# Kernel tuning notes

Hardware: AMD Instinct MI355X
Metric: run time of the kernel (lower is better)

## Reference

```python
import jax, jax.numpy as jnp
import numpy as np

DIM = 384
NUM_HEADS = 12
HEAD_DIM = DIM // NUM_HEADS  # 32
SCALE = HEAD_DIM ** -0.5
B, N = 4, 2048


def setup_inputs() -> dict:
    key = jax.random.key(0)
    k0, k1, k2, k3 = jax.random.split(key, 4)
    x = jax.random.normal(k0, (B, N, DIM), dtype=jnp.float32)
    # nn.Linear(dim, 3*dim, bias=False): y = x @ W_qkv, W_qkv is [C, 3C]
    W_qkv = jax.random.normal(k1, (DIM, 3 * DIM), dtype=jnp.float32) * (DIM ** -0.5)
    # nn.Linear(dim, dim): y = x @ W_proj + b_proj, W_proj is [C, C]
    W_proj = jax.random.normal(k2, (DIM, DIM), dtype=jnp.float32) * (DIM ** -0.5)
    b_proj = jax.random.normal(k3, (DIM,), dtype=jnp.float32) * 0.01
    return {"x": x, "W_qkv": W_qkv, "W_proj": W_proj, "b_proj": b_proj}


def reference(x, W_qkv, W_proj, b_proj):
    b, n, c = x.shape
    qkv = (x @ W_qkv).reshape(b, n, 3, NUM_HEADS, HEAD_DIM)
    qkv = jnp.transpose(qkv, (2, 0, 3, 1, 4))  # [3, B, H, N, hd]
    q, k, v = qkv[0], qkv[1], qkv[2]
    # full attention: softmax(q k^T * scale) v
    attn = jnp.einsum('bhqd,bhkd->bhqk', q, k) * SCALE  # [B,H,N,N]
    attn = jax.nn.softmax(attn, axis=-1)
    out = jnp.einsum('bhqk,bhkd->bhqd', attn, v)  # [B,H,N,hd]
    out = jnp.transpose(out, (0, 2, 1, 3)).reshape(b, n, c)
    return out @ W_proj + b_proj
```

## Files before the change

### kernel.cpp

```cpp
#include <hip/hip_runtime.h>

constexpr int BB  = 4;
constexpr int SEQ = 2048;
constexpr int CC  = 384;
constexpr int C3  = 1152;
constexpr int NH  = 12;
constexpr int HD  = 32;
constexpr float SCALE = 0.17677669529663689f;
constexpr float LOG2E = 1.4426950408889634f;
constexpr size_t KV_BYTES = (size_t)2 * BB * NH * SEQ * HD * 2;
constexpr size_t WT_BYTES = ((size_t)C3 * CC + (size_t)CC * CC) * 2;
constexpr size_t XB_BYTES = (size_t)BB * SEQ * CC * 2;

typedef __attribute__((ext_vector_type(8))) short short8_t;
typedef __attribute__((ext_vector_type(4))) float floatx4;

#if __has_builtin(__builtin_amdgcn_exp2f)
#define EXP2F __builtin_amdgcn_exp2f
#else
#define EXP2F __builtin_exp2f
#endif

__device__ __forceinline__ unsigned short f2bf(float f) {
    unsigned int u = __builtin_bit_cast(unsigned int, f);
    u += 0x7fffu + ((u >> 16) & 1u);
    return (unsigned short)(u >> 16);
}
__device__ __forceinline__ unsigned int pk_rn(float lo, float hi) {
    return __builtin_amdgcn_perm(__builtin_bit_cast(unsigned int, hi) + 0x8000u,
                                 __builtin_bit_cast(unsigned int, lo) + 0x8000u,
                                 0x07060302u);
}
__device__ __forceinline__ short8_t pack8(float4 a, float4 b) {
    uint4 u;
    u.x = pk_rn(a.x, a.y); u.y = pk_rn(a.z, a.w);
    u.z = pk_rn(b.x, b.y); u.w = pk_rn(b.z, b.w);
    return __builtin_bit_cast(short8_t, u);
}

__global__ __launch_bounds__(256) void prep_kernel(
    const float* __restrict__ x, const float* __restrict__ wqkv,
    const float* __restrict__ wproj,
    unsigned short* __restrict__ wqkvT, unsigned short* __restrict__ wprojT,
    unsigned short* __restrict__ xb)
{
    const int bid = blockIdx.x;
    if (bid >= 144) {
        const size_t base = (size_t)(bid - 144) * 2048 + threadIdx.x * 8;
        const float4 a = *(const float4*)(x + base);
        const float4 b = *(const float4*)(x + base + 4);
        uint4 u;
        u.x = pk_rn(a.x, a.y); u.y = pk_rn(a.z, a.w);
        u.z = pk_rn(b.x, b.y); u.w = pk_rn(b.z, b.w);
        *(uint4*)(xb + base) = u;
        return;
    }
    __shared__ float ls[64][68];
    const float* src; unsigned short* dst; int SN, k0, n0;
    if (bid < 108) {
        src = wqkv; dst = wqkvT; SN = C3;
        k0 = (bid / 18) * 64; n0 = (bid % 18) * 64;
    } else {
        const int b2 = bid - 108;
        src = wproj; dst = wprojT; SN = CC;
        k0 = (b2 / 6) * 64; n0 = (b2 % 6) * 64;
    }
    const int t  = threadIdx.x;
    const int rr = t >> 4, cc4 = (t & 15) * 4;
#pragma unroll
    for (int p = 0; p < 4; ++p) {
        const int row = p * 16 + rr;
        const float4 v = *(const float4*)&src[(size_t)(k0 + row) * SN + n0 + cc4];
        ls[row][cc4] = v.x; ls[row][cc4 + 1] = v.y;
        ls[row][cc4 + 2] = v.z; ls[row][cc4 + 3] = v.w;
    }
    __syncthreads();
#pragma unroll
    for (int p = 0; p < 4; ++p) {
        const int nrow = p * 16 + rr;
        uint2 u;
        u.x = pk_rn(ls[cc4][nrow],     ls[cc4 + 1][nrow]);
        u.y = pk_rn(ls[cc4 + 2][nrow], ls[cc4 + 3][nrow]);
        *(uint2*)&dst[(size_t)(n0 + nrow) * CC + k0 + cc4] = u;
    }
}

__global__ __launch_bounds__(256) void qkv_fast(
    const unsigned short* __restrict__ xb,
    const unsigned short* __restrict__ wT,
    float* __restrict__ dq,
    unsigned short* __restrict__ kv)
{
    __shared__ __align__(16) unsigned short As[2][128][40];
    __shared__ __align__(16) unsigned short Bs[2][128][40];

    const int mt   = blockIdx.x & 63;
    const int nb   = blockIdx.x >> 6;
    const int tid  = threadIdx.x;
    const int wid  = tid >> 6;
    const int lane = tid & 63;
    const int quad = lane >> 4;
    const int col  = lane & 15;
    const int wr   = wid >> 1, wc = wid & 1;
    const int m0 = mt * 128, n0 = nb * 128;

    const int arow = tid >> 1;
    const int aoff = (tid & 1) * 16;

    floatx4 acc[4][4];
#pragma unroll
    for (int i = 0; i < 4; ++i)
#pragma unroll
        for (int j = 0; j < 4; ++j) acc[i][j] = (floatx4){0.f, 0.f, 0.f, 0.f};

    const unsigned short* xrow = xb + (size_t)(m0 + arow) * CC + aoff;
    const unsigned short* wrow = wT + (size_t)(n0 + arow) * CC + aoff;

    short8_t ast0, ast1, bst0, bst1;
    ast0 = *(const short8_t*)xrow;
    ast1 = *(const short8_t*)(xrow + 8);
    bst0 = *(const short8_t*)wrow;
    bst1 = *(const short8_t*)(wrow + 8);
    *(short8_t*)&As[0][arow][aoff]     = ast0;
    *(short8_t*)&As[0][arow][aoff + 8] = ast1;
    *(short8_t*)&Bs[0][arow][aoff]     = bst0;
    *(short8_t*)&Bs[0][arow][aoff + 8] = bst1;

    for (int it = 0; it < CC / 32; ++it) {
        const int kn = (it + 1 < CC / 32) ? (it + 1) * 32 : 0;
        ast0 = *(const short8_t*)(xrow + kn);
        ast1 = *(const short8_t*)(xrow + kn + 8);
        bst0 = *(const short8_t*)(wrow + kn);
        bst1 = *(const short8_t*)(wrow + kn + 8);

        __syncthreads();
        const int p = it & 1;
        short8_t af[4], bf[4];
#pragma unroll
        for (int i = 0; i < 4; ++i)
            af[i] = *(const short8_t*)&As[p][wr * 64 + i * 16 + col][quad * 8];
#pragma unroll
        for (int j = 0; j < 4; ++j)
            bf[j] = *(const short8_t*)&Bs[p][wc * 64 + j * 16 + col][quad * 8];
#pragma unroll
        for (int j = 0; j < 4; ++j)
#pragma unroll
            for (int i = 0; i < 4; ++i)
                acc[i][j] = __builtin_amdgcn_mfma_f32_16x16x32_bf16(af[i], bf[j], acc[i][j], 0, 0, 0);

        *(short8_t*)&As[p ^ 1][arow][aoff]     = ast0;
        *(short8_t*)&As[p ^ 1][arow][aoff + 8] = ast1;
        *(short8_t*)&Bs[p ^ 1][arow][aoff]     = bst0;
        *(short8_t*)&Bs[p ^ 1][arow][aoff + 8] = bst1;
    }

    const int t = nb / 3;
#pragma unroll
    for (int i = 0; i < 4; ++i) {
        const int mg = m0 + wr * 64 + i * 16 + quad * 4;
        if (t == 0) {
#pragma unroll
            for (int j = 0; j < 4; ++j) {
                const int n = n0 + wc * 64 + j * 16 + col;
#pragma unroll
                for (int r = 0; r < 4; ++r)
                    dq[(size_t)(mg + r) * CC + n] = acc[i][j][r];
            }
        } else if (t == 1) {
            const int b = mg >> 11, s = mg & (SEQ - 1);
#pragma unroll
            for (int j = 0; j < 4; ++j) {
                const int rem = n0 - CC + wc * 64 + j * 16 + col;
                const int h = rem >> 5, d = rem & 31;
                unsigned short* kp = kv + ((size_t)(b * NH + h) * SEQ + s) * HD + d;
#pragma unroll
                for (int r = 0; r < 4; ++r)
                    kp[(size_t)r * HD] = f2bf(acc[i][j][r]);
            }
        } else {
            const int b = mg >> 11, s = mg & (SEQ - 1);
            unsigned short* vtb = kv + (size_t)BB * NH * SEQ * HD;
#pragma unroll
            for (int j = 0; j < 4; ++j) {
                const int rem = n0 - 2 * CC + wc * 64 + j * 16 + col;
                const int h = rem >> 5, d = rem & 31;
                uint2 u;
                u.x = pk_rn(acc[i][j][0], acc[i][j][1]);
                u.y = pk_rn(acc[i][j][2], acc[i][j][3]);
                *(uint2*)&vtb[((size_t)(b * NH + h) * HD + d) * SEQ + s] = u;
            }
        }
    }
}

__global__ __launch_bounds__(256) void attn_kernel(
    const unsigned short* __restrict__ kv,
    float* qatt)
{
    const int bid  = blockIdx.x;
    const int qp   = bid / 48;
    const int bh   = bid % 48;
    const int h    = bh % NH;
    const int b    = bh / NH;
    const int w    = threadIdx.x >> 6;
    const int lane = threadIdx.x & 63;
    const int quad = lane >> 4;
    const int col  = lane & 15;
    const int tid  = threadIdx.x;

    const unsigned short* K  = kv + (size_t)bh * SEQ * HD;
    const unsigned short* VT = kv + (size_t)BB * NH * SEQ * HD + (size_t)bh * HD * SEQ;

    __shared__ __align__(16) unsigned short Kt[2][128][40];
    __shared__ __align__(16) unsigned short Vt[2][32][136];

    const int krow_s = tid >> 1, koff_s = (tid & 1) * 16;
    const int drow_s = tid >> 3, voff_s = (tid & 7) * 16;

    int qrow[2];
    short8_t qf[2];
    const float sc = SCALE * LOG2E;
#pragma unroll
    for (int t = 0; t < 2; ++t) {
        qrow[t] = b * SEQ + qp * 128 + (w + 4 * t) * 16 + col;
        const float* qpt = qatt + (size_t)qrow[t] * CC + h * HD + quad * 8;
        const float4 a0 = *(const float4*)qpt;
        const float4 a1 = *(const float4*)(qpt + 4);
        const float4 s0 = {a0.x * sc, a0.y * sc, a0.z * sc, a0.w * sc};
        const float4 s1 = {a1.x * sc, a1.y * sc, a1.z * sc, a1.w * sc};
        qf[t] = pack8(s0, s1);
    }

    short8_t ones;
#pragma unroll
    for (int e = 0; e < 8; ++e) ones[e] = (short)0x3F80;

    floatx4 o[2][2];
    floatx4 lacc[2];
#pragma unroll
    for (int t = 0; t < 2; ++t) {
        lacc[t] = (floatx4){0.f, 0.f, 0.f, 0.f};
#pragma unroll
        for (int i = 0; i < 2; ++i) o[t][i] = (floatx4){0.f, 0.f, 0.f, 0.f};
    }
    const float ci = -10.f * LOG2E;
    const floatx4 cinit = {ci, ci, ci, ci};

    short8_t k0a = *(const short8_t*)(K + (size_t)krow_s * HD + koff_s);
    short8_t k0b = *(const short8_t*)(K + (size_t)krow_s * HD + koff_s + 8);
    short8_t v0a = *(const short8_t*)(VT + (size_t)drow_s * SEQ + voff_s);
    short8_t v0b = *(const short8_t*)(VT + (size_t)drow_s * SEQ + voff_s + 8);
    *(short8_t*)&Kt[0][krow_s][koff_s]     = k0a;
    *(short8_t*)&Kt[0][krow_s][koff_s + 8] = k0b;
    *(short8_t*)&Vt[0][drow_s][voff_s]     = v0a;
    *(short8_t*)&Vt[0][drow_s][voff_s + 8] = v0b;

    for (int it = 0; it < SEQ / 128; ++it) {
        const int kn = ((it + 1) * 128) & (SEQ - 1);
        k0a = *(const short8_t*)(K + (size_t)(kn + krow_s) * HD + koff_s);
        k0b = *(const short8_t*)(K + (size_t)(kn + krow_s) * HD + koff_s + 8);
        v0a = *(const short8_t*)(VT + (size_t)drow_s * SEQ + kn + voff_s);
        v0b = *(const short8_t*)(VT + (size_t)drow_s * SEQ + kn + voff_s + 8);

        __syncthreads();
        const int p = it & 1;

#pragma unroll
        for (int c = 0; c < 4; ++c) {
            const int c32 = c * 32;
            const short8_t ka0 = *(const short8_t*)&Kt[p][c32 + col][quad * 8];
            const short8_t ka1 = *(const short8_t*)&Kt[p][c32 + 16 + col][quad * 8];
            const uint2 w0a = *(const uint2*)&Vt[p][col][c32 + quad * 4];
            const uint2 w0b = *(const uint2*)&Vt[p][col][c32 + 16 + quad * 4];
            const uint2 w1a = *(const uint2*)&Vt[p][16 + col][c32 + quad * 4];
            const uint2 w1b = *(const uint2*)&Vt[p][16 + col][c32 + 16 + quad * 4];
            const short8_t va0 = __builtin_bit_cast(short8_t, (uint4){w0a.x, w0a.y, w0b.x, w0b.y});
            const short8_t va1 = __builtin_bit_cast(short8_t, (uint4){w1a.x, w1a.y, w1b.x, w1b.y});
#pragma unroll
            for (int t = 0; t < 2; ++t) {
                const floatx4 s0 = __builtin_amdgcn_mfma_f32_16x16x32_bf16(ka0, qf[t], cinit, 0, 0, 0);
                const floatx4 s1 = __builtin_amdgcn_mfma_f32_16x16x32_bf16(ka1, qf[t], cinit, 0, 0, 0);
                const float p00 = EXP2F(s0[0]), p01 = EXP2F(s0[1]);
                const float p02 = EXP2F(s0[2]), p03 = EXP2F(s0[3]);
                const float p10 = EXP2F(s1[0]), p11 = EXP2F(s1[1]);
                const float p12 = EXP2F(s1[2]), p13 = EXP2F(s1[3]);
                const uint4 pu = {pk_rn(p00, p01), pk_rn(p02, p03),
                                  pk_rn(p10, p11), pk_rn(p12, p13)};
                const short8_t pb = __builtin_bit_cast(short8_t, pu);
                o[t][0] = __builtin_amdgcn_mfma_f32_16x16x32_bf16(va0, pb, o[t][0], 0, 0, 0);
                o[t][1] = __builtin_amdgcn_mfma_f32_16x16x32_bf16(va1, pb, o[t][1], 0, 0, 0);
                lacc[t] = __builtin_amdgcn_mfma_f32_16x16x32_bf16(ones, pb, lacc[t], 0, 0, 0);
            }
        }

        *(short8_t*)&Kt[p ^ 1][krow_s][koff_s]     = k0a;
        *(short8_t*)&Kt[p ^ 1][krow_s][koff_s + 8] = k0b;
        *(short8_t*)&Vt[p ^ 1][drow_s][voff_s]     = v0a;
        *(short8_t*)&Vt[p ^ 1][drow_s][voff_s + 8] = v0b;
    }

#pragma unroll
    for (int t = 0; t < 2; ++t) {
        const float inv = 1.f / lacc[t][0];
        float* op = qatt + (size_t)qrow[t] * CC + h * HD;
#pragma unroll
        for (int r = 0; r < 4; ++r) {
            op[quad * 4 + r]      = o[t][0][r] * inv;
            op[16 + quad * 4 + r] = o[t][1][r] * inv;
        }
    }
}

__global__ __launch_bounds__(256) void proj_fast(
    float* att,
    const unsigned short* __restrict__ wT,
    const float* __restrict__ bias)
{
    __shared__ __align__(16) unsigned short Bs[2][384][32];
    __shared__ __align__(16) unsigned short As[2][32][40];

    const int mt   = blockIdx.x;
    const int tid  = threadIdx.x;
    const int wid  = tid >> 6;
    const int lane = tid & 63;
    const int quad = lane >> 4;
    const int col  = lane & 15;
    const int m0   = mt * 32;

    const int arow = tid >> 3, akoff = (tid & 7) * 4;

    floatx4 acc[2][6];
#pragma unroll
    for (int i = 0; i < 2; ++i)
#pragma unroll
        for (int j = 0; j < 6; ++j) acc[i][j] = (floatx4){0.f, 0.f, 0.f, 0.f};

    short8_t bst[3][2];
    uint2 asr;
    {
#pragma unroll
        for (int j = 0; j < 3; ++j) {
            const int f = j * 256 + tid;
            const unsigned short* wp = wT + (size_t)(f >> 1) * CC + (f & 1) * 16;
            bst[j][0] = *(const short8_t*)wp;
            bst[j][1] = *(const short8_t*)(wp + 8);
        }
        const float4 av = *(const float4*)(att + (size_t)(m0 + arow) * CC + akoff);
        asr = (uint2){pk_rn(av.x, av.y), pk_rn(av.z, av.w)};
#pragma unroll
        for (int j = 0; j < 3; ++j) {
            const int f = j * 256 + tid;
            *(short8_t*)&Bs[0][f >> 1][(f & 1) * 16]     = bst[j][0];
            *(short8_t*)&Bs[0][f >> 1][(f & 1) * 16 + 8] = bst[j][1];
        }
        *(uint2*)&As[0][arow][akoff] = asr;
    }

    for (int it = 0; it < CC / 32; ++it) {
        const int kn = (it + 1 < CC / 32) ? (it + 1) * 32 : 0;
#pragma unroll
        for (int j = 0; j < 3; ++j) {
            const int f = j * 256 + tid;
            const unsigned short* wp = wT + (size_t)(f >> 1) * CC + kn + (f & 1) * 16;
            bst[j][0] = *(const short8_t*)wp;
            bst[j][1] = *(const short8_t*)(wp + 8);
        }
        const float4 av = *(const float4*)(att + (size_t)(m0 + arow) * CC + kn + akoff);
        asr = (uint2){pk_rn(av.x, av.y), pk_rn(av.z, av.w)};

        __syncthreads();
        const int p = it & 1;
        short8_t af[2], bf[6];
#pragma unroll
        for (int i = 0; i < 2; ++i)
            af[i] = *(const short8_t*)&As[p][i * 16 + col][quad * 8];
#pragma unroll
        for (int j = 0; j < 6; ++j)
            bf[j] = *(const short8_t*)&Bs[p][wid * 96 + j * 16 + col][quad * 8];
#pragma unroll
        for (int j = 0; j < 6; ++j)
#pragma unroll
            for (int i = 0; i < 2; ++i)
                acc[i][j] = __builtin_amdgcn_mfma_f32_16x16x32_bf16(af[i], bf[j], acc[i][j], 0, 0, 0);

#pragma unroll
        for (int j = 0; j < 3; ++j) {
            const int f = j * 256 + tid;
            *(short8_t*)&Bs[p ^ 1][f >> 1][(f & 1) * 16]     = bst[j][0];
            *(short8_t*)&Bs[p ^ 1][f >> 1][(f & 1) * 16 + 8] = bst[j][1];
        }
        *(uint2*)&As[p ^ 1][arow][akoff] = asr;
    }

    __syncthreads();
#pragma unroll
    for (int j = 0; j < 6; ++j) {
        const int n = wid * 96 + j * 16 + col;
        const float bv = bias[n];
#pragma unroll
        for (int i = 0; i < 2; ++i)
#pragma unroll
            for (int r = 0; r < 4; ++r)
                att[(size_t)(m0 + i * 16 + quad * 4 + r) * CC + n] = acc[i][j][r] + bv;
    }
}

__global__ __launch_bounds__(256) void qkv_lds(
    const float* __restrict__ x, const float* __restrict__ w,
    float* __restrict__ dq, unsigned short* __restrict__ kv)
{
    __shared__ __align__(16) unsigned short wt[128 * 40];
    const int mt = blockIdx.x & 63, nb = blockIdx.x >> 6;
    const int tid = threadIdx.x, wid = tid >> 6, lane = tid & 63;
    const int quad = lane >> 4, col = lane & 15;
    const int wr = wid >> 1, wc = wid & 1;
    const int m0 = mt * 128, n0 = nb * 128;
    const int sn = tid >> 1, skg = (tid & 1) * 4;

    floatx4 acc[4][4];
#pragma unroll
    for (int i = 0; i < 4; ++i)
#pragma unroll
        for (int j = 0; j < 4; ++j) acc[i][j] = (floatx4){0.f, 0.f, 0.f, 0.f};
    const float* xbase = x + (size_t)(m0 + wr * 64 + col) * CC;

    for (int kb = 0; kb < CC; kb += 32) {
        float wv[4][4];
#pragma unroll
        for (int s = 0; s < 4; ++s) {
            const int k = kb + (skg + s) * 4;
#pragma unroll
            for (int j = 0; j < 4; ++j) wv[s][j] = w[(size_t)(k + j) * C3 + n0 + sn];
        }
        short8_t af[4];
#pragma unroll
        for (int i = 0; i < 4; ++i) {
            const float* xr = xbase + (size_t)i * 16 * CC + kb + quad * 8;
            af[i] = pack8(*(const float4*)xr, *(const float4*)(xr + 4));
        }
        __syncthreads();
#pragma unroll
        for (int s = 0; s < 4; ++s) {
            ushort4 u;
            u.x = f2bf(wv[s][0]); u.y = f2bf(wv[s][1]);
            u.z = f2bf(wv[s][2]); u.w = f2bf(wv[s][3]);
            *(ushort4*)&wt[sn * 40 + (skg + s) * 4] = u;
        }
        __syncthreads();
#pragma unroll
        for (int j = 0; j < 4; ++j) {
            const short8_t bf = *(const short8_t*)&wt[(wc * 64 + j * 16 + col) * 40 + quad * 8];
#pragma unroll
            for (int i = 0; i < 4; ++i)
                acc[i][j] = __builtin_amdgcn_mfma_f32_16x16x32_bf16(af[i], bf, acc[i][j], 0, 0, 0);
        }
    }
    const int t = nb / 3;
#pragma unroll
    for (int i = 0; i < 4; ++i) {
        const int mg = m0 + wr * 64 + i * 16 + quad * 4;
        if (t == 0) {
#pragma unroll
            for (int j = 0; j < 4; ++j) {
                const int n = n0 + wc * 64 + j * 16 + col;
#pragma unroll
                for (int r = 0; r < 4; ++r) dq[(size_t)(mg + r) * CC + n] = acc[i][j][r];
            }
        } else if (t == 1) {
            const int b = mg >> 11, s = mg & (SEQ - 1);
#pragma unroll
            for (int j = 0; j < 4; ++j) {
                const int rem = n0 - CC + wc * 64 + j * 16 + col;
                const int h = rem >> 5, d = rem & 31;
                unsigned short* kp = kv + ((size_t)(b * NH + h) * SEQ + s) * HD + d;
#pragma unroll
                for (int r = 0; r < 4; ++r) kp[(size_t)r * HD] = f2bf(acc[i][j][r]);
            }
        } else {
            const int b = mg >> 11, s = mg & (SEQ - 1);
            unsigned short* vtb = kv + (size_t)BB * NH * SEQ * HD;
#pragma unroll
            for (int j = 0; j < 4; ++j) {
                const int rem = n0 - 2 * CC + wc * 64 + j * 16 + col;
                const int h = rem >> 5, d = rem & 31;
                uint2 u;
                u.x = pk_rn(acc[i][j][0], acc[i][j][1]);
                u.y = pk_rn(acc[i][j][2], acc[i][j][3]);
                *(uint2*)&vtb[((size_t)(b * NH + h) * HD + d) * SEQ + s] = u;
            }
        }
    }
}

__global__ __launch_bounds__(256) void proj_lds(
    float* att, const float* __restrict__ wp, const float* __restrict__ bias)
{
    __shared__ __align__(16) unsigned short wt[CC * 40];
    const int mt = blockIdx.x, tid = threadIdx.x, wid = tid >> 6, lane = tid & 63;
    const int quad = lane >> 4, col = lane & 15;
    const int m0 = mt * 16;
    floatx4 acc[6];
#pragma unroll
    for (int j = 0; j < 6; ++j) acc[j] = (floatx4){0.f, 0.f, 0.f, 0.f};
    for (int kb = 0; kb < CC; kb += 32) {
        float gv[12][4];
#pragma unroll
        for (int g = 0; g < 12; ++g) {
            const int flat = tid + g * 256, n = flat % 384, kg = flat / 384;
#pragma unroll
            for (int j = 0; j < 4; ++j) gv[g][j] = wp[(size_t)(kb + kg * 4 + j) * CC + n];
        }
        __syncthreads();
#pragma unroll
        for (int g = 0; g < 12; ++g) {
            const int flat = tid + g * 256, n = flat % 384, kg = flat / 384;
            ushort4 u;
            u.x = f2bf(gv[g][0]); u.y = f2bf(gv[g][1]);
            u.z = f2bf(gv[g][2]); u.w = f2bf(gv[g][3]);
            *(ushort4*)&wt[n * 40 + kg * 4] = u;
        }
        __syncthreads();
        const float* ap = att + (size_t)(m0 + col) * CC + kb + quad * 8;
        const short8_t af = pack8(*(const float4*)ap, *(const float4*)(ap + 4));
#pragma unroll
        for (int j = 0; j < 6; ++j) {
            const short8_t pb = *(const short8_t*)&wt[(wid * 96 + j * 16 + col) * 40 + quad * 8];
            acc[j] = __builtin_amdgcn_mfma_f32_16x16x32_bf16(af, pb, acc[j], 0, 0, 0);
        }
    }
    __syncthreads();
#pragma unroll
    for (int j = 0; j < 6; ++j) {
        const int n = wid * 96 + j * 16 + col;
        const float bv = bias[n];
#pragma unroll
        for (int r = 0; r < 4; ++r)
            att[(size_t)(m0 + quad * 4 + r) * CC + n] = acc[j][r] + bv;
    }
}

__global__ void marker_kernel(float* out, float val, int nelem) {
    int i = blockIdx.x * 256 + threadIdx.x;
    if (i < nelem) out[i] = val;
}

extern "C" void kernel_launch(void* const* d_in, const int* in_sizes, int n_in,
                              void* d_out, int out_size, void* d_ws, size_t ws_size,
                              hipStream_t stream)
{
    const float* x     = (const float*)d_in[0];
    const float* wqkv  = (const float*)d_in[1];
    const float* wproj = (const float*)d_in[2];
    const float* bproj = (const float*)d_in[3];
    float* out = (float*)d_out;
    unsigned short* kv = (unsigned short*)d_ws;

    if (ws_size < KV_BYTES) {
        const float marker = 100.f + (float)(ws_size >> 20);
        marker_kernel<<<(out_size + 255) / 256, 256, 0, stream>>>(out, marker, out_size);
        return;
    }

    unsigned short* wqkvT  = kv + (size_t)2 * BB * NH * SEQ * HD;
    unsigned short* wprojT = wqkvT + (size_t)C3 * CC;
    unsigned short* xb     = wprojT + (size_t)CC * CC;

    if (ws_size >= KV_BYTES + WT_BYTES + XB_BYTES) {
        prep_kernel<<<144 + 1536, 256, 0, stream>>>(x, wqkv, wproj, wqkvT, wprojT, xb);
        qkv_fast<<<576, 256, 0, stream>>>(xb, wqkvT, out, kv);
        attn_kernel<<<16 * BB * NH, 256, 0, stream>>>(kv, out);
        proj_fast<<<BB * SEQ / 32, 256, 0, stream>>>(out, wprojT, bproj);
    } else {
        qkv_lds<<<576, 256, 0, stream>>>(x, wqkv, out, kv);
        attn_kernel<<<16 * BB * NH, 256, 0, stream>>>(kv, out);
        proj_lds<<<BB * SEQ / 16, 256, 0, stream>>>(out, wproj, bproj);
    }
}
```

Measured before the change: 143.3 us.

## Store Q and attention output as bf16 intermediates, fold softmax scale into K

The QKV GEMM now writes Q as bf16 into the output buffer instead of fp32. The softmax scale is folded into K at write time. The attention kernel reads bf16 Q directly and writes its output as bf16 into the xb workspace, so proj_fast loads A fragments straight from global memory with no LDS staging or fp32-to-bf16 conversion. This halves the intermediate traffic and removes a shared-memory buffer and one barrier, at the cost of rounding Q before the scale is applied and keeping a duplicate fp32 attention kernel for the fallback path.

```diff
diff --git a/kernel.cpp b/kernel.cpp
--- a/kernel.cpp
+++ b/kernel.cpp
@@ -8,6 +8,7 @@
 constexpr int HD  = 32;
 constexpr float SCALE = 0.17677669529663689f;
 constexpr float LOG2E = 1.4426950408889634f;
+constexpr float KSC   = SCALE * LOG2E;
 constexpr size_t KV_BYTES = (size_t)2 * BB * NH * SEQ * HD * 2;
 constexpr size_t WT_BYTES = ((size_t)C3 * CC + (size_t)CC * CC) * 2;
 constexpr size_t XB_BYTES = (size_t)BB * SEQ * CC * 2;
@@ -88,7 +89,7 @@
 __global__ __launch_bounds__(256) void qkv_fast(
     const unsigned short* __restrict__ xb,
     const unsigned short* __restrict__ wT,
-    float* __restrict__ dq,
+    unsigned short* __restrict__ qb,
     unsigned short* __restrict__ kv)
 {
     __shared__ __align__(16) unsigned short As[2][128][40];
@@ -164,7 +165,7 @@
                 const int n = n0 + wc * 64 + j * 16 + col;
 #pragma unroll
                 for (int r = 0; r < 4; ++r)
-                    dq[(size_t)(mg + r) * CC + n] = acc[i][j][r];
+                    qb[(size_t)(mg + r) * CC + n] = f2bf(acc[i][j][r]);
             }
         } else if (t == 1) {
             const int b = mg >> 11, s = mg & (SEQ - 1);
@@ -175,7 +176,7 @@
                 unsigned short* kp = kv + ((size_t)(b * NH + h) * SEQ + s) * HD + d;
 #pragma unroll
                 for (int r = 0; r < 4; ++r)
-                    kp[(size_t)r * HD] = f2bf(acc[i][j][r]);
+                    kp[(size_t)r * HD] = f2bf(acc[i][j][r] * KSC);
             }
         } else {
             const int b = mg >> 11, s = mg & (SEQ - 1);
@@ -195,7 +196,8 @@
 
 __global__ __launch_bounds__(256) void attn_kernel(
     const unsigned short* __restrict__ kv,
-    float* qatt)
+    const unsigned short* __restrict__ qb,
+    unsigned short* __restrict__ ab)
 {
     const int bid  = blockIdx.x;
     const int qp   = bid / 48;
@@ -219,16 +221,10 @@
 
     int qrow[2];
     short8_t qf[2];
-    const float sc = SCALE * LOG2E;
 #pragma unroll
     for (int t = 0; t < 2; ++t) {
         qrow[t] = b * SEQ + qp * 128 + (w + 4 * t) * 16 + col;
-        const float* qpt = qatt + (size_t)qrow[t] * CC + h * HD + quad * 8;
-        const float4 a0 = *(const float4*)qpt;
-        const float4 a1 = *(const float4*)(qpt + 4);
-        const float4 s0 = {a0.x * sc, a0.y * sc, a0.z * sc, a0.w * sc};
-        const float4 s1 = {a1.x * sc, a1.y * sc, a1.z * sc, a1.w * sc};
-        qf[t] = pack8(s0, s1);
+        qf[t] = *(const short8_t*)(qb + (size_t)qrow[t] * CC + h * HD + quad * 8);
     }
 
     short8_t ones;
@@ -302,22 +298,24 @@
 #pragma unroll
     for (int t = 0; t < 2; ++t) {
         const float inv = 1.f / lacc[t][0];
-        float* op = qatt + (size_t)qrow[t] * CC + h * HD;
-#pragma unroll
-        for (int r = 0; r < 4; ++r) {
-            op[quad * 4 + r]      = o[t][0][r] * inv;
-            op[16 + quad * 4 + r] = o[t][1][r] * inv;
+        unsigned short* op = ab + (size_t)qrow[t] * CC + h * HD;
+#pragma unroll
+        for (int i = 0; i < 2; ++i) {
+            uint2 u;
+            u.x = pk_rn(o[t][i][0] * inv, o[t][i][1] * inv);
+            u.y = pk_rn(o[t][i][2] * inv, o[t][i][3] * inv);
+            *(uint2*)&op[i * 16 + quad * 4] = u;
         }
     }
 }
 
 __global__ __launch_bounds__(256) void proj_fast(
-    float* att,
+    const unsigned short* __restrict__ ab,
     const unsigned short* __restrict__ wT,
-    const float* __restrict__ bias)
+    const float* __restrict__ bias,
+    float* __restrict__ out)
 {
     __shared__ __align__(16) unsigned short Bs[2][384][32];
-    __shared__ __align__(16) unsigned short As[2][32][40];
 
     const int mt   = blockIdx.x;
     const int tid  = threadIdx.x;
@@ -327,16 +325,17 @@
     const int col  = lane & 15;
     const int m0   = mt * 32;
 
-    const int arow = tid >> 3, akoff = (tid & 7) * 4;
-
     floatx4 acc[2][6];
 #pragma unroll
     for (int i = 0; i < 2; ++i)
 #pragma unroll
         for (int j = 0; j < 6; ++j) acc[i][j] = (floatx4){0.f, 0.f, 0.f, 0.f};
 
+    const unsigned short* arow0 = ab + (size_t)(m0 + col) * CC + quad * 8;
+    const unsigned short* arow1 = arow0 + (size_t)16 * CC;
+
     short8_t bst[3][2];
-    uint2 asr;
+    short8_t af0, af1;
     {
 #pragma unroll
         for (int j = 0; j < 3; ++j) {
@@ -345,15 +344,14 @@
             bst[j][0] = *(const short8_t*)wp;
             bst[j][1] = *(const short8_t*)(wp + 8);
         }
-        const float4 av = *(const float4*)(att + (size_t)(m0 + arow) * CC + akoff);
-        asr = (uint2){pk_rn(av.x, av.y), pk_rn(av.z, av.w)};
+        af0 = *(const short8_t*)arow0;
+        af1 = *(const short8_t*)arow1;
 #pragma unroll
         for (int j = 0; j < 3; ++j) {
             const int f = j * 256 + tid;
             *(short8_t*)&Bs[0][f >> 1][(f & 1) * 16]     = bst[j][0];
             *(short8_t*)&Bs[0][f >> 1][(f & 1) * 16 + 8] = bst[j][1];
         }
-        *(uint2*)&As[0][arow][akoff] = asr;
     }
 
     for (int it = 0; it < CC / 32; ++it) {
@@ -365,23 +363,20 @@
             bst[j][0] = *(const short8_t*)wp;
             bst[j][1] = *(const short8_t*)(wp + 8);
         }
-        const float4 av = *(const float4*)(att + (size_t)(m0 + arow) * CC + kn + akoff);
-        asr = (uint2){pk_rn(av.x, av.y), pk_rn(av.z, av.w)};
+        const short8_t afn0 = *(const short8_t*)(arow0 + kn);
+        const short8_t afn1 = *(const short8_t*)(arow1 + kn);
 
         __syncthreads();
         const int p = it & 1;
-        short8_t af[2], bf[6];
-#pragma unroll
-        for (int i = 0; i < 2; ++i)
-            af[i] = *(const short8_t*)&As[p][i * 16 + col][quad * 8];
+        short8_t bf[6];
 #pragma unroll
         for (int j = 0; j < 6; ++j)
             bf[j] = *(const short8_t*)&Bs[p][wid * 96 + j * 16 + col][quad * 8];
 #pragma unroll
-        for (int j = 0; j < 6; ++j)
-#pragma unroll
-            for (int i = 0; i < 2; ++i)
-                acc[i][j] = __builtin_amdgcn_mfma_f32_16x16x32_bf16(af[i], bf[j], acc[i][j], 0, 0, 0);
+        for (int j = 0; j < 6; ++j) {
+            acc[0][j] = __builtin_amdgcn_mfma_f32_16x16x32_bf16(af0, bf[j], acc[0][j], 0, 0, 0);
+            acc[1][j] = __builtin_amdgcn_mfma_f32_16x16x32_bf16(af1, bf[j], acc[1][j], 0, 0, 0);
+        }
 
 #pragma unroll
         for (int j = 0; j < 3; ++j) {
@@ -389,10 +384,9 @@
             *(short8_t*)&Bs[p ^ 1][f >> 1][(f & 1) * 16]     = bst[j][0];
             *(short8_t*)&Bs[p ^ 1][f >> 1][(f & 1) * 16 + 8] = bst[j][1];
         }
-        *(uint2*)&As[p ^ 1][arow][akoff] = asr;
-    }
-
-    __syncthreads();
+        af0 = afn0; af1 = afn1;
+    }
+
 #pragma unroll
     for (int j = 0; j < 6; ++j) {
         const int n = wid * 96 + j * 16 + col;
@@ -401,7 +395,7 @@
         for (int i = 0; i < 2; ++i)
 #pragma unroll
             for (int r = 0; r < 4; ++r)
-                att[(size_t)(m0 + i * 16 + quad * 4 + r) * CC + n] = acc[i][j][r] + bv;
+                out[(size_t)(m0 + i * 16 + quad * 4 + r) * CC + n] = acc[i][j][r] + bv;
     }
 }
 
@@ -492,6 +486,124 @@
     }
 }
 
+__global__ __launch_bounds__(256) void attn_f32(
+    const unsigned short* __restrict__ kv,
+    float* qatt)
+{
+    const int bid  = blockIdx.x;
+    const int qp   = bid / 48;
+    const int bh   = bid % 48;
+    const int h    = bh % NH;
+    const int b    = bh / NH;
+    const int w    = threadIdx.x >> 6;
+    const int lane = threadIdx.x & 63;
+    const int quad = lane >> 4;
+    const int col  = lane & 15;
+    const int tid  = threadIdx.x;
+
+    const unsigned short* K  = kv + (size_t)bh * SEQ * HD;
+    const unsigned short* VT = kv + (size_t)BB * NH * SEQ * HD + (size_t)bh * HD * SEQ;
+
+    __shared__ __align__(16) unsigned short Kt[2][128][40];
+    __shared__ __align__(16) unsigned short Vt[2][32][136];
+
+    const int krow_s = tid >> 1, koff_s = (tid & 1) * 16;
+    const int drow_s = tid >> 3, voff_s = (tid & 7) * 16;
+
+    int qrow[2];
+    short8_t qf[2];
+    const float sc = SCALE * LOG2E;
+#pragma unroll
+    for (int t = 0; t < 2; ++t) {
+        qrow[t] = b * SEQ + qp * 128 + (w + 4 * t) * 16 + col;
+        const float* qpt = qatt + (size_t)qrow[t] * CC + h * HD + quad * 8;
+        const float4 a0 = *(const float4*)qpt;
+        const float4 a1 = *(const float4*)(qpt + 4);
+        const float4 s0 = {a0.x * sc, a0.y * sc, a0.z * sc, a0.w * sc};
+        const float4 s1 = {a1.x * sc, a1.y * sc, a1.z * sc, a1.w * sc};
+        qf[t] = pack8(s0, s1);
+    }
+
+    short8_t ones;
+#pragma unroll
+    for (int e = 0; e < 8; ++e) ones[e] = (short)0x3F80;
+
+    floatx4 o[2][2];
+    floatx4 lacc[2];
+#pragma unroll
+    for (int t = 0; t < 2; ++t) {
+        lacc[t] = (floatx4){0.f, 0.f, 0.f, 0.f};
+#pragma unroll
+        for (int i = 0; i < 2; ++i) o[t][i] = (floatx4){0.f, 0.f, 0.f, 0.f};
+    }
+    const float ci = -10.f * LOG2E;
+    const floatx4 cinit = {ci, ci, ci, ci};
+
+    short8_t k0a = *(const short8_t*)(K + (size_t)krow_s * HD + koff_s);
+    short8_t k0b = *(const short8_t*)(K + (size_t)krow_s * HD + koff_s + 8);
+    short8_t v0a = *(const short8_t*)(VT + (size_t)drow_s * SEQ + voff_s);
+    short8_t v0b = *(const short8_t*)(VT + (size_t)drow_s * SEQ + voff_s + 8);
+    *(short8_t*)&Kt[0][krow_s][koff_s]     = k0a;
+    *(short8_t*)&Kt[0][krow_s][koff_s + 8] = k0b;
+    *(short8_t*)&Vt[0][drow_s][voff_s]     = v0a;
+    *(short8_t*)&Vt[0][drow_s][voff_s + 8] = v0b;
+
+    for (int it = 0; it < SEQ / 128; ++it) {
+        const int kn = ((it + 1) * 128) & (SEQ - 1);
+        k0a = *(const short8_t*)(K + (size_t)(kn + krow_s) * HD + koff_s);
+        k0b = *(const short8_t*)(K + (size_t)(kn + krow_s) * HD + koff_s + 8);
+        v0a = *(const short8_t*)(VT + (size_t)drow_s * SEQ + kn + voff_s);
+        v0b = *(const short8_t*)(VT + (size_t)drow_s * SEQ + kn + voff_s + 8);
+
+        __syncthreads();
+        const int p = it & 1;
+
+#pragma unroll
+        for (int c = 0; c < 4; ++c) {
+            const int c32 = c * 32;
+            const short8_t ka0 = *(const short8_t*)&Kt[p][c32 + col][quad * 8];
+            const short8_t ka1 = *(const short8_t*)&Kt[p][c32 + 16 + col][quad * 8];
+            const uint2 w0a = *(const uint2*)&Vt[p][col][c32 + quad * 4];
+            const uint2 w0b = *(const uint2*)&Vt[p][col][c32 + 16 + quad * 4];
+            const uint2 w1a = *(const uint2*)&Vt[p][16 + col][c32 + quad * 4];
+            const uint2 w1b = *(const uint2*)&Vt[p][16 + col][c32 + 16 + quad * 4];
+            const short8_t va0 = __builtin_bit_cast(short8_t, (uint4){w0a.x, w0a.y, w0b.x, w0b.y});
+            const short8_t va1 = __builtin_bit_cast(short8_t, (uint4){w1a.x, w1a.y, w1b.x, w1b.y});
+#pragma unroll
+            for (int t = 0; t < 2; ++t) {
+                const floatx4 s0 = __builtin_amdgcn_mfma_f32_16x16x32_bf16(ka0, qf[t], cinit, 0, 0, 0);
+                const floatx4 s1 = __builtin_amdgcn_mfma_f32_16x16x32_bf16(ka1, qf[t], cinit, 0, 0, 0);
+                const float p00 = EXP2F(s0[0]), p01 = EXP2F(s0[1]);
+                const float p02 = EXP2F(s0[2]), p03 = EXP2F(s0[3]);
+                const float p10 = EXP2F(s1[0]), p11 = EXP2F(s1[1]);
+                const float p12 = EXP2F(s1[2]), p13 = EXP2F(s1[3]);
+                const uint4 pu = {pk_rn(p00, p01), pk_rn(p02, p03),
+                                  pk_rn(p10, p11), pk_rn(p12, p13)};
+                const short8_t pb = __builtin_bit_cast(short8_t, pu);
+                o[t][0] = __builtin_amdgcn_mfma_f32_16x16x32_bf16(va0, pb, o[t][0], 0, 0, 0);
+                o[t][1] = __builtin_amdgcn_mfma_f32_16x16x32_bf16(va1, pb, o[t][1], 0, 0, 0);
+                lacc[t] = __builtin_amdgcn_mfma_f32_16x16x32_bf16(ones, pb, lacc[t], 0, 0, 0);
+            }
+        }
+
+        *(short8_t*)&Kt[p ^ 1][krow_s][koff_s]     = k0a;
+        *(short8_t*)&Kt[p ^ 1][krow_s][koff_s + 8] = k0b;
+        *(short8_t*)&Vt[p ^ 1][drow_s][voff_s]     = v0a;
+        *(short8_t*)&Vt[p ^ 1][drow_s][voff_s + 8] = v0b;
+    }
+
+#pragma unroll
+    for (int t = 0; t < 2; ++t) {
+        const float inv = 1.f / lacc[t][0];
+        float* op = qatt + (size_t)qrow[t] * CC + h * HD;
+#pragma unroll
+        for (int r = 0; r < 4; ++r) {
+            op[quad * 4 + r]      = o[t][0][r] * inv;
+            op[16 + quad * 4 + r] = o[t][1][r] * inv;
+        }
+    }
+}
+
 __global__ __launch_bounds__(256) void proj_lds(
     float* att, const float* __restrict__ wp, const float* __restrict__ bias)
 {
@@ -566,13 +678,14 @@
     unsigned short* xb     = wprojT + (size_t)CC * CC;
 
     if (ws_size >= KV_BYTES + WT_BYTES + XB_BYTES) {
+        unsigned short* qb = (unsigned short*)d_out;
         prep_kernel<<<144 + 1536, 256, 0, stream>>>(x, wqkv, wproj, wqkvT, wprojT, xb);
-        qkv_fast<<<576, 256, 0, stream>>>(xb, wqkvT, out, kv);
-        attn_kernel<<<16 * BB * NH, 256, 0, stream>>>(kv, out);
-        proj_fast<<<BB * SEQ / 32, 256, 0, stream>>>(out, wprojT, bproj);
+        qkv_fast<<<576, 256, 0, stream>>>(xb, wqkvT, qb, kv);
+        attn_kernel<<<16 * BB * NH, 256, 0, stream>>>(kv, qb, xb );
+        proj_fast<<<BB * SEQ / 32, 256, 0, stream>>>(xb, wprojT, bproj, out);
     } else {
         qkv_lds<<<576, 256, 0, stream>>>(x, wqkv, out, kv);
-        attn_kernel<<<16 * BB * NH, 256, 0, stream>>>(kv, out);
+        attn_f32<<<16 * BB * NH, 256, 0, stream>>>(kv, out);
         proj_lds<<<BB * SEQ / 16, 256, 0, stream>>>(out, wproj, bproj);
     }
 }
```

After: 141.7 us. No clear change (-1.1%).
